# Kernel optimization log

Hardware: AMD Instinct MI355X
Metric: run time of the kernel (lower is better)

## Reference

```python
import jax, jax.numpy as jnp
import numpy as np

B, H, T = 16, 1024, 4096
CD, CS = 8, 1024  # codebook_dim, codebook_size


def setup_inputs() -> dict:
    key = jax.random.key(0)
    ks = jax.random.split(key, 6)
    return {
        "hidden_state": jax.random.normal(ks[0], (B, H, T), dtype=jnp.float32),
        "in_proj_w": jax.random.normal(ks[1], (CD, H), dtype=jnp.float32) * 0.02,
        "in_proj_b": jax.random.normal(ks[2], (CD,), dtype=jnp.float32) * 0.02,
        "out_proj_w": jax.random.normal(ks[3], (H, CD), dtype=jnp.float32) * 0.02,
        "out_proj_b": jax.random.normal(ks[4], (H,), dtype=jnp.float32) * 0.02,
        "codebook": jax.random.normal(ks[5], (CS, CD), dtype=jnp.float32),
    }


def _l2_normalize(x, axis=-1, eps=1e-12):
    n = jnp.sqrt(jnp.sum(x * x, axis=axis, keepdims=True))
    return x / jnp.maximum(n, eps)


def reference(hidden_state, in_proj_w, in_proj_b, out_proj_w, out_proj_b, codebook):
    sg = jax.lax.stop_gradient
    # 1x1 conv == pointwise linear over channels: [B,H,T] -> [B,CD,T]
    proj = jnp.einsum("bht,dh->bdt", hidden_state, in_proj_w) + in_proj_b[None, :, None]

    # decode_latents: cosine-similarity nearest neighbor
    b, d, t = proj.shape
    enc = proj.transpose(0, 2, 1).reshape(b * t, d)          # [BT, CD]
    enc_n = _l2_normalize(enc, axis=1)
    cb_n = _l2_normalize(codebook, axis=1)                   # [CS, CD]
    l2 = jnp.sum(enc_n * enc_n, axis=1, keepdims=True)       # [BT, 1]
    dist = -(l2 - 2.0 * (enc_n @ cb_n.T)) + jnp.sum(cb_n * cb_n, axis=1)[None, :]
    indices = jnp.argmax(dist, axis=1).reshape(b, t)         # [B, T] int
    quant = codebook[indices].transpose(0, 2, 1)             # [B, CD, T]

    commitment_loss = jnp.mean((proj - sg(quant)) ** 2)
    codebook_loss = jnp.mean((quant - sg(proj)) ** 2)

    # straight-through estimator
    q_st = proj + sg(quant - proj)
    out = jnp.einsum("bdt,hd->bht", q_st, out_proj_w) + out_proj_b[None, :, None]
    return (out, commitment_loss, codebook_loss, indices, proj)
```

## Files before the change

### kernel.cpp

```cpp
#include <hip/hip_runtime.h>
#include <math.h>

#define NB 16
#define NH 1024
#define NT 4096
#define CD 8
#define CS 1024
#define NBT (NB*NT)

__global__ __launch_bounds__(256) void k0_prep(
    const float* __restrict__ w,
    const float* __restrict__ bias,
    const float* __restrict__ cb,
    double* __restrict__ Wt,
    double* __restrict__ biasd,
    double* __restrict__ cbn,
    double* __restrict__ cbn2,
    double* __restrict__ lossacc)
{
    int g = blockIdx.x * 256 + threadIdx.x;
    if (g < CD * NH) {
        int h = g >> 3, d = g & 7;
        Wt[g] = (double)w[d * NH + h];
    }
    if (g < CS) {
        double v[CD];
        double s = 0.0;
        #pragma unroll
        for (int j = 0; j < CD; j++) { v[j] = (double)cb[g * CD + j]; s += v[j] * v[j]; }
        double n = sqrt(s);
        double m = fmax(n, 1e-12);
        double s2 = 0.0;
        #pragma unroll
        for (int j = 0; j < CD; j++) {
            double q = v[j] / m;
            cbn[g * CD + j] = q;
            s2 += q * q;
        }
        cbn2[g] = s2;
    }
    if (g < CD) biasd[g] = (double)bias[g];
    if (g == 0) *lossacc = 0.0;
}

__global__ __launch_bounds__(512) void k1_proj(
    const float*  __restrict__ x,
    const double* __restrict__ Wt,
    const double* __restrict__ biasd,
    double* __restrict__ projd,
    float*  __restrict__ projf)
{
    __shared__ double red[CD][8][64];
    const int tx = threadIdx.x;
    const int ty = threadIdx.y;
    const int bt = blockIdx.x * 64 + tx;
    const int b  = bt >> 12;
    const int t  = bt & (NT - 1);
    const float* xp = x + ((size_t)b * NH) * NT + t;
    const int h0 = __builtin_amdgcn_readfirstlane(ty * 128);

    double acc[CD];
    #pragma unroll
    for (int d = 0; d < CD; d++) acc[d] = 0.0;

    for (int i = 0; i < 128; i += 16) {
        float xv[16];
        #pragma unroll
        for (int j = 0; j < 16; j++) xv[j] = xp[(size_t)(h0 + i + j) * NT];
        #pragma unroll
        for (int j = 0; j < 16; j++) {
            const double xd = (double)xv[j];
            const double* wr = Wt + (h0 + i + j) * CD;
            #pragma unroll
            for (int d = 0; d < CD; d++) acc[d] = fma(xd, wr[d], acc[d]);
        }
    }

    #pragma unroll
    for (int d = 0; d < CD; d++) red[d][ty][tx] = acc[d];
    __syncthreads();

    if (ty == 0) {
        #pragma unroll
        for (int d = 0; d < CD; d++) {
            double s = 0.0;
            #pragma unroll
            for (int j = 0; j < 8; j++) s += red[d][j][tx];
            s += biasd[d];
            projd[(size_t)bt * CD + d] = s;
            projf[((size_t)b * CD + d) * NT + t] = (float)s;
        }
    }
}

__global__ __launch_bounds__(512) void k2_argmax(
    const double* __restrict__ projd,
    const double* __restrict__ cbn,
    const double* __restrict__ cbn2,
    const float*  __restrict__ cb,
    float* __restrict__ idxf,
    int*   __restrict__ idxi,
    double* __restrict__ lossacc)
{
    __shared__ double bestv_s[8][64];
    __shared__ int    besti_s[8][64];
    const int tx = threadIdx.x;
    const int ty = threadIdx.y;
    const int bt = blockIdx.x * 64 + tx;

    double p[CD];
    #pragma unroll
    for (int d = 0; d < CD; d++) p[d] = projd[(size_t)bt * CD + d];

    double s = 0.0;
    #pragma unroll
    for (int d = 0; d < CD; d++) s += p[d] * p[d];
    const double m = fmax(sqrt(s), 1e-12);
    double pn2[CD];
    #pragma unroll
    for (int d = 0; d < CD; d++) pn2[d] = 2.0 * (p[d] / m);

    const int c0 = __builtin_amdgcn_readfirstlane(ty * 128);
    double best = -1e300;
    int bi = 0;
    #pragma unroll 4
    for (int c = 0; c < 128; c++) {
        const double* cr = cbn + (size_t)(c0 + c) * CD;
        double dot = cbn2[c0 + c];
        #pragma unroll
        for (int d = 0; d < CD; d++) dot = fma(pn2[d], cr[d], dot);
        if (dot > best) { best = dot; bi = c; }
    }
    bestv_s[ty][tx] = best;
    besti_s[ty][tx] = c0 + bi;
    __syncthreads();

    if (ty == 0) {
        double bv = bestv_s[0][tx];
        int    bc = besti_s[0][tx];
        #pragma unroll
        for (int j = 1; j < 8; j++) {
            const double v = bestv_s[j][tx];
            const int    c = besti_s[j][tx];
            if (v > bv) { bv = v; bc = c; }
        }
        idxf[bt] = (float)bc;
        idxi[bt] = bc;

        const float* qr = cb + (size_t)bc * CD;
        double ls = 0.0;
        #pragma unroll
        for (int d = 0; d < CD; d++) {
            const float pf = (float)p[d];
            const float df = pf - qr[d];
            const float sq = df * df;
            ls += (double)sq;
        }
        #pragma unroll
        for (int o = 32; o > 0; o >>= 1) ls += __shfl_down(ls, o, 64);
        if (tx == 0) atomicAdd(lossacc, ls);
    }
}

__global__ __launch_bounds__(512) void k4_out(
    const double* __restrict__ projd,
    const int*    __restrict__ idxi,
    const float*  __restrict__ cb,
    const float*  __restrict__ wo,
    const float*  __restrict__ bo,
    const double* __restrict__ lossacc,
    float* __restrict__ out,
    float* __restrict__ lossout)
{
    if (blockIdx.x == 0 && threadIdx.x == 0 && threadIdx.y == 0) {
        const float v = (float)(*lossacc / (double)(NB * CD * NT));
        lossout[0] = v;
        lossout[1] = v;
    }

    const int tx = threadIdx.x;
    const int ty = threadIdx.y;
    const int bt = blockIdx.x * 64 + tx;
    const int b  = bt >> 12;
    const int t  = bt & (NT - 1);

    const int bi = idxi[bt];
    float q[CD];
    #pragma unroll
    for (int d = 0; d < CD; d++) {
        const float pf = (float)projd[(size_t)bt * CD + d];
        const float cf = cb[(size_t)bi * CD + d];
        q[d] = pf + (cf - pf);
    }

    const int h0 = __builtin_amdgcn_readfirstlane(ty * 128);
    float* op = out + ((size_t)b * NH) * NT + t;

    #pragma unroll 4
    for (int i = 0; i < 128; i++) {
        const int h = h0 + i;
        const float* wr = wo + (size_t)h * CD;
        float o = 0.f;
        #pragma unroll
        for (int d = 0; d < CD; d++) o = fmaf(q[d], wr[d], o);
        o += bo[h];
        op[(size_t)h * NT] = o;
    }
}

extern "C" void kernel_launch(void* const* d_in, const int* in_sizes, int n_in,
                              void* d_out, int out_size, void* d_ws, size_t ws_size,
                              hipStream_t stream) {
    const float* hidden = (const float*)d_in[0];
    const float* ipw    = (const float*)d_in[1];
    const float* ipb    = (const float*)d_in[2];
    const float* opw    = (const float*)d_in[3];
    const float* opb    = (const float*)d_in[4];
    const float* cb     = (const float*)d_in[5];

    float* out      = (float*)d_out;
    float* loss_out = out + (size_t)NB * NH * NT;
    float* idxf     = loss_out + 2;
    float* projf    = idxf + NBT;

    double* Wt      = (double*)d_ws;
    double* biasd   = Wt + CD * NH;
    double* cbn     = biasd + 8;
    double* cbn2    = cbn + (size_t)CS * CD;
    double* lossacc = cbn2 + CS;
    double* projd   = lossacc + 8;
    int*    idxi    = (int*)(projd + (size_t)NBT * CD);

    k0_prep<<<32, 256, 0, stream>>>(ipw, ipb, cb, Wt, biasd, cbn, cbn2, lossacc);
    k1_proj<<<NBT / 64, dim3(64, 8), 0, stream>>>(hidden, Wt, biasd, projd, projf);
    k2_argmax<<<NBT / 64, dim3(64, 8), 0, stream>>>(projd, cbn, cbn2, cb, idxf, idxi, lossacc);
    k4_out<<<NBT / 64, dim3(64, 8), 0, stream>>>(projd, idxi, cb, opw, opb, lossacc, out, loss_out);
}
```

Before: 540.6 us.

## Fuse projection, argmax and output into one kernel with fp32 argmax and fp64 fallback

Merges the projection, nearest-codebook search and output-projection kernels into one fused kernel of 128 tokens per block, which keeps projections in shared memory instead of round-tripping through global memory. The codebook search now runs in fp32 and tracks the top-two scores, re-running an exact fp64 search only for rows whose margin falls under a threshold. Loss finalisation moves to a last-block-done counter. This trades the global traffic of three kernels and the fp64 argmax cost for more shared memory, extra synchronisation and a heuristic precision fallback.

After: 564.9 us. 1.04x slower.

```diff
diff --git a/kernel.cpp b/kernel.cpp
--- a/kernel.cpp
+++ b/kernel.cpp
@@ -7,6 +7,9 @@
 #define CD 8
 #define CS 1024
 #define NBT (NB*NT)
+#define TPB 128
+#define GRID (NBT/TPB)
+#define MARGIN 1e-3f
 
 __global__ __launch_bounds__(256) void k0_prep(
     const float* __restrict__ w,
@@ -16,7 +19,10 @@
     double* __restrict__ biasd,
     double* __restrict__ cbn,
     double* __restrict__ cbn2,
-    double* __restrict__ lossacc)
+    float*  __restrict__ cbnf,
+    float*  __restrict__ cbn2f,
+    double* __restrict__ lossacc,
+    unsigned* __restrict__ donecnt)
 {
     int g = blockIdx.x * 256 + threadIdx.x;
     if (g < CD * NH) {
@@ -35,176 +41,253 @@
         for (int j = 0; j < CD; j++) {
             double q = v[j] / m;
             cbn[g * CD + j] = q;
+            cbnf[g * CD + j] = (float)q;
             s2 += q * q;
         }
         cbn2[g] = s2;
+        cbn2f[g] = (float)s2;
     }
     if (g < CD) biasd[g] = (double)bias[g];
-    if (g == 0) *lossacc = 0.0;
+    if (g == 0) { *lossacc = 0.0; *donecnt = 0u; }
 }
 
-__global__ __launch_bounds__(512) void k1_proj(
+struct __align__(16) Smem {
+    double projs[TPB][CD];
+    union {
+        double red[8][64][2][4];
+        struct {
+            float  pn2f[TPB][CD];
+            float  bv4[4][TPB];
+            float  sv4[4][TPB];
+            int    bi4[4][TPB];
+            int    bfin[TPB];
+            int    flag[TPB];
+            float  qf[TPB][CD];
+        } b;
+    } u;
+};
+
+__global__ __launch_bounds__(512) void k_fused(
     const float*  __restrict__ x,
     const double* __restrict__ Wt,
     const double* __restrict__ biasd,
-    double* __restrict__ projd,
-    float*  __restrict__ projf)
-{
-    __shared__ double red[CD][8][64];
-    const int tx = threadIdx.x;
-    const int ty = threadIdx.y;
-    const int bt = blockIdx.x * 64 + tx;
-    const int b  = bt >> 12;
-    const int t  = bt & (NT - 1);
-    const float* xp = x + ((size_t)b * NH) * NT + t;
-    const int h0 = __builtin_amdgcn_readfirstlane(ty * 128);
-
-    double acc[CD];
-    #pragma unroll
-    for (int d = 0; d < CD; d++) acc[d] = 0.0;
-
-    for (int i = 0; i < 128; i += 16) {
-        float xv[16];
-        #pragma unroll
-        for (int j = 0; j < 16; j++) xv[j] = xp[(size_t)(h0 + i + j) * NT];
-        #pragma unroll
-        for (int j = 0; j < 16; j++) {
-            const double xd = (double)xv[j];
-            const double* wr = Wt + (h0 + i + j) * CD;
-            #pragma unroll
-            for (int d = 0; d < CD; d++) acc[d] = fma(xd, wr[d], acc[d]);
-        }
-    }
-
-    #pragma unroll
-    for (int d = 0; d < CD; d++) red[d][ty][tx] = acc[d];
-    __syncthreads();
-
-    if (ty == 0) {
-        #pragma unroll
-        for (int d = 0; d < CD; d++) {
-            double s = 0.0;
-            #pragma unroll
-            for (int j = 0; j < 8; j++) s += red[d][j][tx];
-            s += biasd[d];
-            projd[(size_t)bt * CD + d] = s;
-            projf[((size_t)b * CD + d) * NT + t] = (float)s;
-        }
-    }
-}
-
-__global__ __launch_bounds__(512) void k2_argmax(
-    const double* __restrict__ projd,
     const double* __restrict__ cbn,
     const double* __restrict__ cbn2,
-    const float*  __restrict__ cb,
-    float* __restrict__ idxf,
-    int*   __restrict__ idxi,
-    double* __restrict__ lossacc)
-{
-    __shared__ double bestv_s[8][64];
-    __shared__ int    besti_s[8][64];
-    const int tx = threadIdx.x;
-    const int ty = threadIdx.y;
-    const int bt = blockIdx.x * 64 + tx;
-
-    double p[CD];
-    #pragma unroll
-    for (int d = 0; d < CD; d++) p[d] = projd[(size_t)bt * CD + d];
-
-    double s = 0.0;
-    #pragma unroll
-    for (int d = 0; d < CD; d++) s += p[d] * p[d];
-    const double m = fmax(sqrt(s), 1e-12);
-    double pn2[CD];
-    #pragma unroll
-    for (int d = 0; d < CD; d++) pn2[d] = 2.0 * (p[d] / m);
-
-    const int c0 = __builtin_amdgcn_readfirstlane(ty * 128);
-    double best = -1e300;
-    int bi = 0;
-    #pragma unroll 4
-    for (int c = 0; c < 128; c++) {
-        const double* cr = cbn + (size_t)(c0 + c) * CD;
-        double dot = cbn2[c0 + c];
-        #pragma unroll
-        for (int d = 0; d < CD; d++) dot = fma(pn2[d], cr[d], dot);
-        if (dot > best) { best = dot; bi = c; }
-    }
-    bestv_s[ty][tx] = best;
-    besti_s[ty][tx] = c0 + bi;
-    __syncthreads();
-
-    if (ty == 0) {
-        double bv = bestv_s[0][tx];
-        int    bc = besti_s[0][tx];
-        #pragma unroll
-        for (int j = 1; j < 8; j++) {
-            const double v = bestv_s[j][tx];
-            const int    c = besti_s[j][tx];
-            if (v > bv) { bv = v; bc = c; }
-        }
-        idxf[bt] = (float)bc;
-        idxi[bt] = bc;
-
-        const float* qr = cb + (size_t)bc * CD;
-        double ls = 0.0;
-        #pragma unroll
-        for (int d = 0; d < CD; d++) {
-            const float pf = (float)p[d];
-            const float df = pf - qr[d];
-            const float sq = df * df;
-            ls += (double)sq;
-        }
-        #pragma unroll
-        for (int o = 32; o > 0; o >>= 1) ls += __shfl_down(ls, o, 64);
-        if (tx == 0) atomicAdd(lossacc, ls);
-    }
-}
-
-__global__ __launch_bounds__(512) void k4_out(
-    const double* __restrict__ projd,
-    const int*    __restrict__ idxi,
+    const float*  __restrict__ cbnf,
+    const float*  __restrict__ cbn2f,
     const float*  __restrict__ cb,
     const float*  __restrict__ wo,
     const float*  __restrict__ bo,
-    const double* __restrict__ lossacc,
+    double* __restrict__ lossacc,
+    unsigned* __restrict__ donecnt,
     float* __restrict__ out,
-    float* __restrict__ lossout)
+    float* __restrict__ lossout,
+    float* __restrict__ idxf,
+    float* __restrict__ projf)
 {
-    if (blockIdx.x == 0 && threadIdx.x == 0 && threadIdx.y == 0) {
-        const float v = (float)(*lossacc / (double)(NB * CD * NT));
-        lossout[0] = v;
-        lossout[1] = v;
-    }
-
-    const int tx = threadIdx.x;
-    const int ty = threadIdx.y;
-    const int bt = blockIdx.x * 64 + tx;
-    const int b  = bt >> 12;
-    const int t  = bt & (NT - 1);
-
-    const int bi = idxi[bt];
-    float q[CD];
+    __shared__ Smem sm;
+    const int tx  = threadIdx.x;
+    const int ty  = threadIdx.y;
+    const int tid = ty * 64 + tx;
+    const int bt0 = blockIdx.x * TPB;
+    const int b   = bt0 >> 12;
+    const int t0  = bt0 & (NT - 1);
+
+    const int h0 = __builtin_amdgcn_readfirstlane(ty * 128);
+    const float* xp = x + ((size_t)b * NH) * NT + t0 + tx * 2;
+
+    double acc[2][CD];
+    #pragma unroll
+    for (int tt = 0; tt < 2; tt++)
+        #pragma unroll
+        for (int d = 0; d < CD; d++) acc[tt][d] = 0.0;
+
+    for (int i = 0; i < 128; i += 8) {
+        float2 xv[8];
+        #pragma unroll
+        for (int j = 0; j < 8; j++) xv[j] = *(const float2*)(xp + (size_t)(h0 + i + j) * NT);
+        #pragma unroll
+        for (int j = 0; j < 8; j++) {
+            const double* wr = Wt + (size_t)(h0 + i + j) * CD;
+            const double x0 = (double)xv[j].x;
+            const double x1 = (double)xv[j].y;
+            #pragma unroll
+            for (int d = 0; d < CD; d++) {
+                acc[0][d] = fma(x0, wr[d], acc[0][d]);
+                acc[1][d] = fma(x1, wr[d], acc[1][d]);
+            }
+        }
+    }
+
+    const int tl = tid & (TPB - 1);
+    const int dg = __builtin_amdgcn_readfirstlane(tid >> 7);
+
+    #pragma unroll
+    for (int tt = 0; tt < 2; tt++)
+        #pragma unroll
+        for (int dd = 0; dd < 4; dd++) sm.u.red[ty][tx][tt][dd] = acc[tt][dd];
+    __syncthreads();
+    {
+        const int d = dg;
+        double s = 0.0;
+        #pragma unroll
+        for (int j = 0; j < 8; j++) s += sm.u.red[j][tl >> 1][tl & 1][dg];
+        s += biasd[d];
+        sm.projs[tl][d] = s;
+        projf[((size_t)b * CD + d) * NT + t0 + tl] = (float)s;
+    }
+    __syncthreads();
+    #pragma unroll
+    for (int tt = 0; tt < 2; tt++)
+        #pragma unroll
+        for (int dd = 0; dd < 4; dd++) sm.u.red[ty][tx][tt][dd] = acc[tt][4 + dd];
+    __syncthreads();
+    {
+        const int d = 4 + dg;
+        double s = 0.0;
+        #pragma unroll
+        for (int j = 0; j < 8; j++) s += sm.u.red[j][tl >> 1][tl & 1][dg];
+        s += biasd[d];
+        sm.projs[tl][d] = s;
+        projf[((size_t)b * CD + d) * NT + t0 + tl] = (float)s;
+    }
+    __syncthreads();
+
+    if (tid < TPB) {
+        double p[CD];
+        double s = 0.0;
+        #pragma unroll
+        for (int d = 0; d < CD; d++) { p[d] = sm.projs[tid][d]; s += p[d] * p[d]; }
+        const double m = fmax(sqrt(s), 1e-12);
+        #pragma unroll
+        for (int d = 0; d < CD; d++) sm.u.b.pn2f[tid][d] = (float)(2.0 * (p[d] / m));
+    }
+    __syncthreads();
+
+    {
+        const int r = tid & (TPB - 1);
+        const int cc = tid >> 7;
+        const int cbase = __builtin_amdgcn_readfirstlane(cc * 256);
+        float pn[CD];
+        #pragma unroll
+        for (int d = 0; d < CD; d++) pn[d] = sm.u.b.pn2f[r][d];
+        float best = -3.4e38f, second = -3.4e38f;
+        int bidx = cbase;
+        #pragma unroll 4
+        for (int c = 0; c < 256; c++) {
+            const float* cr = cbnf + (size_t)(cbase + c) * CD;
+            float dot = cbn2f[cbase + c];
+            #pragma unroll
+            for (int d = 0; d < CD; d++) dot = fmaf(pn[d], cr[d], dot);
+            second = fmaxf(second, fminf(dot, best));
+            if (dot > best) { best = dot; bidx = cbase + c; }
+        }
+        sm.u.b.bv4[cc][r] = best;
+        sm.u.b.sv4[cc][r] = second;
+        sm.u.b.bi4[cc][r] = bidx;
+    }
+    __syncthreads();
+
+    if (tid < TPB) {
+        float bv = sm.u.b.bv4[0][tid];
+        float sv = sm.u.b.sv4[0][tid];
+        int   bi = sm.u.b.bi4[0][tid];
+        #pragma unroll
+        for (int k = 1; k < 4; k++) {
+            const float bk = sm.u.b.bv4[k][tid];
+            const float sk = sm.u.b.sv4[k][tid];
+            const int   ik = sm.u.b.bi4[k][tid];
+            sv = fmaxf(fmaxf(sv, sk), fminf(bv, bk));
+            if (bk > bv) { bv = bk; bi = ik; }
+        }
+        sm.u.b.bfin[tid] = bi;
+        sm.u.b.flag[tid] = (bv - sv <= MARGIN) ? 1 : 0;
+    }
+    __syncthreads();
+
+    for (int rr = 0; rr < 16; rr++) {
+        const int r = ty * 16 + rr;
+        if (sm.u.b.flag[r]) {
+            double p[CD];
+            double s = 0.0;
+            #pragma unroll
+            for (int d = 0; d < CD; d++) { p[d] = sm.projs[r][d]; s += p[d] * p[d]; }
+            const double m = fmax(sqrt(s), 1e-12);
+            double pn[CD];
+            #pragma unroll
+            for (int d = 0; d < CD; d++) pn[d] = 2.0 * (p[d] / m);
+            double best = -1e300;
+            int bidx = 0;
+            for (int k = 0; k < 16; k++) {
+                const int c = k * 64 + tx;
+                const double* cr = cbn + (size_t)c * CD;
+                double dot = cbn2[c];
+                #pragma unroll
+                for (int d = 0; d < CD; d++) dot = fma(pn[d], cr[d], dot);
+                if (dot > best) { best = dot; bidx = c; }
+            }
+            #pragma unroll
+            for (int off = 32; off; off >>= 1) {
+                const double ov = __shfl_xor(best, off, 64);
+                const int    oi = __shfl_xor(bidx, off, 64);
+                if (ov > best || (ov == best && oi < bidx)) { best = ov; bidx = oi; }
+            }
+            if (tx == 0) sm.u.b.bfin[r] = bidx;
+        }
+    }
+    __syncthreads();
+
+    if (tid < TPB) {
+        const int r = tid;
+        const int bi = sm.u.b.bfin[r];
+        idxf[bt0 + r] = (float)bi;
+        const float* qr = cb + (size_t)bi * CD;
+        double ls = 0.0;
+        #pragma unroll
+        for (int d = 0; d < CD; d++) {
+            const float pf = (float)sm.projs[r][d];
+            const float cf = qr[d];
+            sm.u.b.qf[r][d] = pf + (cf - pf);
+            const float df = pf - cf;
+            ls += (double)(df * df);
+        }
+        #pragma unroll
+        for (int off = 32; off; off >>= 1) ls += __shfl_xor(ls, off, 64);
+        if (tx == 0) atomicAdd(lossacc, ls);
+    }
+    __syncthreads();
+
+    float q0[CD], q1[CD];
     #pragma unroll
     for (int d = 0; d < CD; d++) {
-        const float pf = (float)projd[(size_t)bt * CD + d];
-        const float cf = cb[(size_t)bi * CD + d];
-        q[d] = pf + (cf - pf);
-    }
-
-    const int h0 = __builtin_amdgcn_readfirstlane(ty * 128);
-    float* op = out + ((size_t)b * NH) * NT + t;
-
+        q0[d] = sm.u.b.qf[tx * 2][d];
+        q1[d] = sm.u.b.qf[tx * 2 + 1][d];
+    }
+    float* op = out + ((size_t)b * NH) * NT + t0 + tx * 2;
     #pragma unroll 4
     for (int i = 0; i < 128; i++) {
         const int h = h0 + i;
         const float* wr = wo + (size_t)h * CD;
-        float o = 0.f;
-        #pragma unroll
-        for (int d = 0; d < CD; d++) o = fmaf(q[d], wr[d], o);
-        o += bo[h];
-        op[(size_t)h * NT] = o;
+        float o0 = 0.f, o1 = 0.f;
+        #pragma unroll
+        for (int d = 0; d < CD; d++) {
+            o0 = fmaf(q0[d], wr[d], o0);
+            o1 = fmaf(q1[d], wr[d], o1);
+        }
+        const float bh = bo[h];
+        o0 += bh; o1 += bh;
+        *(float2*)(op + (size_t)h * NT) = make_float2(o0, o1);
+    }
+
+    if (tid == 0) {
+        __threadfence();
+        const unsigned v = atomicAdd(donecnt, 1u);
+        if (v == GRID - 1) {
+            const double tot = atomicAdd(lossacc, 0.0);
+            const float lv = (float)(tot / (double)((size_t)NB * CD * NT));
+            lossout[0] = lv;
+            lossout[1] = lv;
+        }
     }
 }
 
@@ -228,11 +311,13 @@
     double* cbn     = biasd + 8;
     double* cbn2    = cbn + (size_t)CS * CD;
     double* lossacc = cbn2 + CS;
-    double* projd   = lossacc + 8;
-    int*    idxi    = (int*)(projd + (size_t)NBT * CD);
-
-    k0_prep<<<32, 256, 0, stream>>>(ipw, ipb, cb, Wt, biasd, cbn, cbn2, lossacc);
-    k1_proj<<<NBT / 64, dim3(64, 8), 0, stream>>>(hidden, Wt, biasd, projd, projf);
-    k2_argmax<<<NBT / 64, dim3(64, 8), 0, stream>>>(projd, cbn, cbn2, cb, idxf, idxi, lossacc);
-    k4_out<<<NBT / 64, dim3(64, 8), 0, stream>>>(projd, idxi, cb, opw, opb, lossacc, out, loss_out);
+    float*  cbnf    = (float*)(lossacc + 8);
+    float*  cbn2f   = cbnf + (size_t)CS * CD;
+    unsigned* donecnt = (unsigned*)(cbn2f + CS);
+
+    k0_prep<<<32, 256, 0, stream>>>(ipw, ipb, cb, Wt, biasd, cbn, cbn2, cbnf, cbn2f,
+                                    lossacc, donecnt);
+    k_fused<<<GRID, dim3(64, 8), 0, stream>>>(hidden, Wt, biasd, cbn, cbn2, cbnf, cbn2f,
+                                              cb, opw, opb, lossacc, donecnt,
+                                              out, loss_out, idxf, projf);
 }
```
